# Kernel tuning notes

Hardware: AMD Instinct MI355X
Metric: run time of the kernel (lower is better)

## Reference

```python
import jax, jax.numpy as jnp
import numpy as np
import math

CODE_DIMS = [32, 32]
NUM_CODEBOOK = 16
FEAT_DIM = 1024
EPS = 1e-12


def rms_norm(x, eps=EPS):
    var = jnp.mean(x * x, axis=-1, keepdims=True) + eps
    return x * jax.lax.rsqrt(var)


def outer_product(y, code_dims):
    # y: [..., h, sum(code_dims)] -> [..., h, prod(code_dims)]
    splits = list(np.cumsum(code_dims)[:-1])
    mats = jnp.split(y, splits, axis=-1)
    out = mats[0]
    for m in mats[1:]:
        out = out[..., :, None] * m[..., None, :]
        out = out.reshape(*out.shape[:-2], -1)
    return out


def setup_inputs() -> dict:
    key = jax.random.key(0)
    kx, kw = jax.random.split(key)
    x = jax.random.normal(kx, (4, 2048, FEAT_DIM), dtype=jnp.float32)
    std = math.sqrt(2.0 / (FEAT_DIM + sum(CODE_DIMS)))
    weight = jax.random.normal(kw, (NUM_CODEBOOK, FEAT_DIM, sum(CODE_DIMS)), dtype=jnp.float32) * std
    return {"x": x, "weight": weight}


def reference(x, weight):
    h = weight.shape[0]
    # batched per-codebook linear: [..., d] x [h, d, o] -> [..., h, o]
    y = jnp.einsum('...i,hio->...ho', x, weight)
    # chunked outer product per codebook -> [..., h, prod(code_dims)]
    op = outer_product(y, CODE_DIMS)
    out = jnp.mean(op, axis=-2) * math.sqrt(h)
    return rms_norm(out)
```

## Files before the change

### kernel.cpp

```cpp
#include <hip/hip_runtime.h>
#include <hip/hip_bf16.h>

#define KDIM  1024
#define NOUT  1024
#define NTOK  8192
#define NCB   16
#define BM    256
#define BN    128
#define BK    64
#define BUFSZ 49152
#define NBUF  3

typedef __attribute__((ext_vector_type(8))) short short8;
typedef __attribute__((ext_vector_type(4))) float f32x4;

__device__ static inline unsigned short f2bf(float f) {
    unsigned int u = __float_as_uint(f);
    return (unsigned short)((u + 0x7FFFu + ((u >> 16) & 1u)) >> 16);
}

__device__ static inline float bf2f(unsigned int h) {
    return __uint_as_float(h << 16);
}

__device__ static inline void async_copy16(const void* g, void* l) {
    __builtin_amdgcn_global_load_lds(
        (const __attribute__((address_space(1))) void*)g,
        (__attribute__((address_space(3))) void*)l, 16, 0, 0);
}

__global__ __launch_bounds__(256) void conv_x_kernel(const float* __restrict__ x,
                                                     unsigned short* __restrict__ A) {
    int u = blockIdx.x * 256 + threadIdx.x;
    const float* src = x + (size_t)u * 8;
    float4 v0 = *(const float4*)(src);
    float4 v1 = *(const float4*)(src + 4);
    short8 o;
    o[0] = (short)f2bf(v0.x); o[1] = (short)f2bf(v0.y);
    o[2] = (short)f2bf(v0.z); o[3] = (short)f2bf(v0.w);
    o[4] = (short)f2bf(v1.x); o[5] = (short)f2bf(v1.y);
    o[6] = (short)f2bf(v1.z); o[7] = (short)f2bf(v1.w);
    *(short8*)(A + (size_t)u * 8) = o;
}

__global__ __launch_bounds__(256) void conv_w_kernel(const float* __restrict__ W,
                                                     unsigned short* __restrict__ Bt) {
    int u = blockIdx.x * 256 + threadIdx.x;
    int n  = u & (NOUT - 1);
    int k0 = (u >> 10) << 3;
    int h = n >> 6, o = n & 63;
    const float* src = W + (size_t)h * KDIM * 64 + o;
    short8 v;
#pragma unroll
    for (int j = 0; j < 8; ++j)
        v[j] = (short)f2bf(src[(size_t)(k0 + j) * 64]);
    *(short8*)(Bt + (size_t)n * KDIM + k0) = v;
}

__device__ __forceinline__ void stage_tile(const unsigned short* __restrict__ A,
                                           const unsigned short* __restrict__ Bt,
                                           char* lbase, int tid, int m0, int n0, int kel) {
    unsigned short* Al = (unsigned short*)lbase;
    unsigned short* Bl = (unsigned short*)(lbase + 32768);
#pragma unroll
    for (int i = 0; i < 4; ++i) {
        int s = i * 512 + tid;
        int row = s >> 3;
        int cs = (s & 7) ^ (row & 7);
        async_copy16(A + (size_t)(m0 + row) * KDIM + kel + cs * 8, Al + s * 8);
    }
#pragma unroll
    for (int i = 0; i < 2; ++i) {
        int s = i * 512 + tid;
        int row = s >> 3;
        int cs = (s & 7) ^ (row & 7);
        async_copy16(Bt + (size_t)(n0 + row) * KDIM + kel + cs * 8, Bl + s * 8);
    }
}

template <int VM, bool DO_STAGE>
__device__ __forceinline__ void gemm_step(const unsigned short* __restrict__ A,
                                          const unsigned short* __restrict__ Bt,
                                          char* lds, int tid, int m0, int n0, int kt,
                                          int wm, int wn, int r15, int q,
                                          f32x4 (&acc)[4][4]) {
    if (DO_STAGE)
        stage_tile(A, Bt, lds + ((kt + 2) % NBUF) * BUFSZ, tid, m0, n0, (kt + 2) * BK);
    asm volatile("s_waitcnt vmcnt(%0)" :: "i"(VM) : "memory");
    __builtin_amdgcn_sched_barrier(0);
    __builtin_amdgcn_s_barrier();

    const unsigned short* Al = (const unsigned short*)(lds + (kt % NBUF) * BUFSZ);
    const unsigned short* Bl = (const unsigned short*)(lds + (kt % NBUF) * BUFSZ + 32768);
    short8 af[4][2], bf[4][2];
#pragma unroll
    for (int mf = 0; mf < 4; ++mf)
#pragma unroll
        for (int kk = 0; kk < 2; ++kk) {
            int row = wm * 64 + mf * 16 + r15;
            int c = kk * 4 + q;
            af[mf][kk] = *(const short8*)(Al + row * 64 + ((c ^ (row & 7)) << 3));
        }
#pragma unroll
    for (int nf = 0; nf < 4; ++nf)
#pragma unroll
        for (int kk = 0; kk < 2; ++kk) {
            int row = wn * 64 + nf * 16 + r15;
            int c = kk * 4 + q;
            bf[nf][kk] = *(const short8*)(Bl + row * 64 + ((c ^ (row & 7)) << 3));
        }
    asm volatile("s_waitcnt lgkmcnt(0)" ::: "memory");
    __builtin_amdgcn_sched_barrier(0);
    __builtin_amdgcn_s_barrier();

    __builtin_amdgcn_s_setprio(1);
#pragma unroll
    for (int kk = 0; kk < 2; ++kk)
#pragma unroll
        for (int mf = 0; mf < 4; ++mf)
#pragma unroll
            for (int nf = 0; nf < 4; ++nf)
                acc[mf][nf] = __builtin_amdgcn_mfma_f32_16x16x32_bf16(af[mf][kk], bf[nf][kk], acc[mf][nf], 0, 0, 0);
    __builtin_amdgcn_s_setprio(0);
}

__global__ __launch_bounds__(512, 2) void gemm_kernel(const unsigned short* __restrict__ A,
                                                      const unsigned short* __restrict__ Bt,
                                                      unsigned short* __restrict__ Y) {
    extern __shared__ char lds[];

    const int id  = blockIdx.x;
    const int xcd = id & 7;
    const int j   = id >> 3;
    const int m0  = (xcd * 4 + (j >> 3)) * BM;
    const int n0  = (j & 7) * BN;

    const int tid  = threadIdx.x;
    const int lane = tid & 63;
    const int w    = tid >> 6;
    const int wm   = w >> 1;
    const int wn   = w & 1;
    const int r15  = lane & 15;
    const int q    = lane >> 4;

    f32x4 acc[4][4];
#pragma unroll
    for (int mf = 0; mf < 4; ++mf)
#pragma unroll
        for (int nf = 0; nf < 4; ++nf)
            acc[mf][nf] = (f32x4){0.f, 0.f, 0.f, 0.f};

    stage_tile(A, Bt, lds,         tid, m0, n0, 0);
    stage_tile(A, Bt, lds + BUFSZ, tid, m0, n0, BK);

    for (int kt = 0; kt < 14; ++kt)
        gemm_step<12, true>(A, Bt, lds, tid, m0, n0, kt, wm, wn, r15, q, acc);
    gemm_step<6, false>(A, Bt, lds, tid, m0, n0, 14, wm, wn, r15, q, acc);
    gemm_step<0, false>(A, Bt, lds, tid, m0, n0, 15, wm, wn, r15, q, acc);

#pragma unroll
    for (int mf = 0; mf < 4; ++mf)
#pragma unroll
        for (int nf = 0; nf < 4; ++nf) {
            int col = n0 + wn * 64 + nf * 16 + r15;
#pragma unroll
            for (int r = 0; r < 4; ++r) {
                int row = m0 + wm * 64 + mf * 16 + q * 4 + r;
                Y[(size_t)row * NOUT + col] = f2bf(acc[mf][nf][r]);
            }
        }
}

__global__ __launch_bounds__(256) void epilogue_kernel(const unsigned short* __restrict__ Y,
                                                       float* __restrict__ out) {
    __shared__ float ylds[1024];
    __shared__ float red[4];

    const int t = blockIdx.x;
    const int tid = threadIdx.x;
    const unsigned short* yrow = Y + (size_t)t * NOUT;

    {
        uint2 raw = *(const uint2*)(yrow + tid * 4);
        ylds[tid * 4 + 0] = bf2f(raw.x & 0xffffu);
        ylds[tid * 4 + 1] = bf2f(raw.x >> 16);
        ylds[tid * 4 + 2] = bf2f(raw.y & 0xffffu);
        ylds[tid * 4 + 3] = bf2f(raw.y >> 16);
    }
    __syncthreads();

    const int jj = tid >> 3;
    const int k0 = (tid & 7) * 4;

    float o0 = 0.f, o1 = 0.f, o2 = 0.f, o3 = 0.f;
#pragma unroll
    for (int h = 0; h < NCB; ++h) {
        float a = ylds[h * 64 + jj];
        float4 bb = *(const float4*)&ylds[h * 64 + 32 + k0];
        o0 += a * bb.x; o1 += a * bb.y; o2 += a * bb.z; o3 += a * bb.w;
    }
    o0 *= 0.25f; o1 *= 0.25f; o2 *= 0.25f; o3 *= 0.25f;

    float ss = o0 * o0 + o1 * o1 + o2 * o2 + o3 * o3;
#pragma unroll
    for (int off = 32; off >= 1; off >>= 1)
        ss += __shfl_xor(ss, off, 64);

    const int lane = tid & 63, wv = tid >> 6;
    if (lane == 0) red[wv] = ss;
    __syncthreads();
    float tot = red[0] + red[1] + red[2] + red[3];
    float scale = rsqrtf(tot * (1.0f / 1024.0f) + 1e-12f);

    float4 o;
    o.x = o0 * scale; o.y = o1 * scale; o.z = o2 * scale; o.w = o3 * scale;
    *(float4*)(out + (size_t)t * 1024 + tid * 4) = o;
}

extern "C" void kernel_launch(void* const* d_in, const int* in_sizes, int n_in,
                              void* d_out, int out_size, void* d_ws, size_t ws_size,
                              hipStream_t stream) {
    const float* x   = (const float*)d_in[0];
    const float* wgt = (const float*)d_in[1];
    float* out = (float*)d_out;

    unsigned short* A  = (unsigned short*)d_ws;
    unsigned short* Bt = (unsigned short*)((char*)d_ws + (16u << 20));
    unsigned short* Y  = (unsigned short*)((char*)d_ws + (18u << 20));

    (void)hipFuncSetAttribute((const void*)gemm_kernel,
                              hipFuncAttributeMaxDynamicSharedMemorySize, NBUF * BUFSZ);

    conv_x_kernel<<<NTOK * KDIM / 8 / 256, 256, 0, stream>>>(x, A);
    conv_w_kernel<<<NOUT * KDIM / 8 / 256, 256, 0, stream>>>(wgt, Bt);
    gemm_kernel<<<(NTOK / BM) * (NOUT / BN), 512, NBUF * BUFSZ, stream>>>(A, Bt, Y);
    epilogue_kernel<<<NTOK, 256, 0, stream>>>(Y, out);
}
```

Before: 49.94 us.

## Fuse fp32-to-bf16 conversion of x into GEMM A-tile staging

```diff
diff --git a/kernel.cpp b/kernel.cpp
--- a/kernel.cpp
+++ b/kernel.cpp
@@ -23,24 +23,15 @@
     return __uint_as_float(h << 16);
 }
 
+__device__ static inline unsigned int pk_bf16(float a, float b) {
+    __hip_bfloat162 h = __float22bfloat162_rn(float2{a, b});
+    return *reinterpret_cast<unsigned int*>(&h);
+}
+
 __device__ static inline void async_copy16(const void* g, void* l) {
     __builtin_amdgcn_global_load_lds(
         (const __attribute__((address_space(1))) void*)g,
         (__attribute__((address_space(3))) void*)l, 16, 0, 0);
-}
-
-__global__ __launch_bounds__(256) void conv_x_kernel(const float* __restrict__ x,
-                                                     unsigned short* __restrict__ A) {
-    int u = blockIdx.x * 256 + threadIdx.x;
-    const float* src = x + (size_t)u * 8;
-    float4 v0 = *(const float4*)(src);
-    float4 v1 = *(const float4*)(src + 4);
-    short8 o;
-    o[0] = (short)f2bf(v0.x); o[1] = (short)f2bf(v0.y);
-    o[2] = (short)f2bf(v0.z); o[3] = (short)f2bf(v0.w);
-    o[4] = (short)f2bf(v1.x); o[5] = (short)f2bf(v1.y);
-    o[6] = (short)f2bf(v1.z); o[7] = (short)f2bf(v1.w);
-    *(short8*)(A + (size_t)u * 8) = o;
 }
 
 __global__ __launch_bounds__(256) void conv_w_kernel(const float* __restrict__ W,
@@ -57,18 +48,9 @@
     *(short8*)(Bt + (size_t)n * KDIM + k0) = v;
 }
 
-__device__ __forceinline__ void stage_tile(const unsigned short* __restrict__ A,
-                                           const unsigned short* __restrict__ Bt,
-                                           char* lbase, int tid, int m0, int n0, int kel) {
-    unsigned short* Al = (unsigned short*)lbase;
+__device__ __forceinline__ void stage_b(const unsigned short* __restrict__ Bt,
+                                        char* lbase, int tid, int n0, int kel) {
     unsigned short* Bl = (unsigned short*)(lbase + 32768);
-#pragma unroll
-    for (int i = 0; i < 4; ++i) {
-        int s = i * 512 + tid;
-        int row = s >> 3;
-        int cs = (s & 7) ^ (row & 7);
-        async_copy16(A + (size_t)(m0 + row) * KDIM + kel + cs * 8, Al + s * 8);
-    }
 #pragma unroll
     for (int i = 0; i < 2; ++i) {
         int s = i * 512 + tid;
@@ -78,17 +60,44 @@
     }
 }
 
-template <int VM, bool DO_STAGE>
-__device__ __forceinline__ void gemm_step(const unsigned short* __restrict__ A,
+__device__ __forceinline__ void load_x(const float* __restrict__ x, int tid,
+                                       int m0, int kel, float4 (&rx)[8]) {
+#pragma unroll
+    for (int i = 0; i < 8; ++i) {
+        int idx = i * 512 + tid;
+        int row = idx >> 4, c = idx & 15;
+        rx[i] = *(const float4*)(x + (size_t)(m0 + row) * KDIM + kel + c * 4);
+    }
+}
+
+__device__ __forceinline__ void write_a(char* lbase, int tid, float4 (&rx)[8]) {
+    unsigned short* Al = (unsigned short*)lbase;
+#pragma unroll
+    for (int i = 0; i < 8; ++i) {
+        int idx = i * 512 + tid;
+        int row = idx >> 4, c = idx & 15;
+        uint2 v;
+        v.x = pk_bf16(rx[i].x, rx[i].y);
+        v.y = pk_bf16(rx[i].z, rx[i].w);
+        *(uint2*)(Al + row * 64 + (((c >> 1) ^ (row & 7)) << 3) + ((c & 1) << 2)) = v;
+    }
+}
+
+template <int VM, bool STAGE, bool CONSUME>
+__device__ __forceinline__ void gemm_step(const float* __restrict__ x,
                                           const unsigned short* __restrict__ Bt,
                                           char* lds, int tid, int m0, int n0, int kt,
                                           int wm, int wn, int r15, int q,
+                                          float4 (&rx_fill)[8], float4 (&rx_cons)[8],
                                           f32x4 (&acc)[4][4]) {
-    if (DO_STAGE)
-        stage_tile(A, Bt, lds + ((kt + 2) % NBUF) * BUFSZ, tid, m0, n0, (kt + 2) * BK);
+    if (STAGE) {
+        load_x(x, tid, m0, (kt + 2) * BK, rx_fill);
+        stage_b(Bt, lds + ((kt + 2) % NBUF) * BUFSZ, tid, n0, (kt + 2) * BK);
+    }
     asm volatile("s_waitcnt vmcnt(%0)" :: "i"(VM) : "memory");
     __builtin_amdgcn_sched_barrier(0);
     __builtin_amdgcn_s_barrier();
+    __builtin_amdgcn_sched_barrier(0);
 
     const unsigned short* Al = (const unsigned short*)(lds + (kt % NBUF) * BUFSZ);
     const unsigned short* Bl = (const unsigned short*)(lds + (kt % NBUF) * BUFSZ + 32768);
@@ -109,9 +118,13 @@
             int c = kk * 4 + q;
             bf[nf][kk] = *(const short8*)(Bl + row * 64 + ((c ^ (row & 7)) << 3));
         }
+    if (CONSUME)
+        write_a(lds + ((kt + 1) % NBUF) * BUFSZ, tid, rx_cons);
+
     asm volatile("s_waitcnt lgkmcnt(0)" ::: "memory");
     __builtin_amdgcn_sched_barrier(0);
     __builtin_amdgcn_s_barrier();
+    __builtin_amdgcn_sched_barrier(0);
 
     __builtin_amdgcn_s_setprio(1);
 #pragma unroll
@@ -124,7 +137,7 @@
     __builtin_amdgcn_s_setprio(0);
 }
 
-__global__ __launch_bounds__(512, 2) void gemm_kernel(const unsigned short* __restrict__ A,
+__global__ __launch_bounds__(512, 2) void gemm_kernel(const float* __restrict__ x,
                                                       const unsigned short* __restrict__ Bt,
                                                       unsigned short* __restrict__ Y) {
     extern __shared__ char lds[];
@@ -150,13 +163,26 @@
         for (int nf = 0; nf < 4; ++nf)
             acc[mf][nf] = (f32x4){0.f, 0.f, 0.f, 0.f};
 
-    stage_tile(A, Bt, lds,         tid, m0, n0, 0);
-    stage_tile(A, Bt, lds + BUFSZ, tid, m0, n0, BK);
-
-    for (int kt = 0; kt < 14; ++kt)
-        gemm_step<12, true>(A, Bt, lds, tid, m0, n0, kt, wm, wn, r15, q, acc);
-    gemm_step<6, false>(A, Bt, lds, tid, m0, n0, 14, wm, wn, r15, q, acc);
-    gemm_step<0, false>(A, Bt, lds, tid, m0, n0, 15, wm, wn, r15, q, acc);
+    float4 rxA[8], rxB[8];
+
+    load_x(x, tid, m0, 0, rxA);
+    stage_b(Bt, lds, tid, n0, 0);
+    asm volatile("s_waitcnt vmcnt(2)" ::: "memory");
+    __builtin_amdgcn_sched_barrier(0);
+    write_a(lds, tid, rxA);
+    load_x(x, tid, m0, BK, rxB);
+    stage_b(Bt, lds + BUFSZ, tid, n0, BK);
+    asm volatile("s_waitcnt lgkmcnt(0)" ::: "memory");
+    __builtin_amdgcn_sched_barrier(0);
+    __builtin_amdgcn_s_barrier();
+
+#pragma unroll 1
+    for (int t2 = 0; t2 < 7; ++t2) {
+        gemm_step<12, true, true>(x, Bt, lds, tid, m0, n0, 2 * t2,     wm, wn, r15, q, rxA, rxB, acc);
+        gemm_step<12, true, true>(x, Bt, lds, tid, m0, n0, 2 * t2 + 1, wm, wn, r15, q, rxB, rxA, acc);
+    }
+    gemm_step<2, false, true >(x, Bt, lds, tid, m0, n0, 14, wm, wn, r15, q, rxA, rxB, acc);
+    gemm_step<0, false, false>(x, Bt, lds, tid, m0, n0, 15, wm, wn, r15, q, rxA, rxA, acc);
 
 #pragma unroll
     for (int mf = 0; mf < 4; ++mf)
@@ -224,15 +250,13 @@
     const float* wgt = (const float*)d_in[1];
     float* out = (float*)d_out;
 
-    unsigned short* A  = (unsigned short*)d_ws;
-    unsigned short* Bt = (unsigned short*)((char*)d_ws + (16u << 20));
-    unsigned short* Y  = (unsigned short*)((char*)d_ws + (18u << 20));
+    unsigned short* Bt = (unsigned short*)d_ws;
+    unsigned short* Y  = (unsigned short*)((char*)d_ws + (2u << 20));
 
     (void)hipFuncSetAttribute((const void*)gemm_kernel,
                               hipFuncAttributeMaxDynamicSharedMemorySize, NBUF * BUFSZ);
 
-    conv_x_kernel<<<NTOK * KDIM / 8 / 256, 256, 0, stream>>>(x, A);
     conv_w_kernel<<<NOUT * KDIM / 8 / 256, 256, 0, stream>>>(wgt, Bt);
-    gemm_kernel<<<(NTOK / BM) * (NOUT / BN), 512, NBUF * BUFSZ, stream>>>(A, Bt, Y);
+    gemm_kernel<<<(NTOK / BM) * (NOUT / BN), 512, NBUF * BUFSZ, stream>>>(x, Bt, Y);
     epilogue_kernel<<<NTOK, 256, 0, stream>>>(Y, out);
 }
```

Measured after the change: 55.00 us. 10.1% more time.

## Shrink GEMM tiles to 128x128x32 with 256 threads and fuse conversion kernels

Applied to the files above, without the earlier changes.

```diff
diff --git a/kernel.cpp b/kernel.cpp
--- a/kernel.cpp
+++ b/kernel.cpp
@@ -5,10 +5,10 @@
 #define NOUT  1024
 #define NTOK  8192
 #define NCB   16
-#define BM    256
+#define BM    128
 #define BN    128
-#define BK    64
-#define BUFSZ 49152
+#define BK    32
+#define TILEB 16384
 #define NBUF  3
 
 typedef __attribute__((ext_vector_type(8))) short short8;
@@ -29,102 +29,91 @@
         (__attribute__((address_space(3))) void*)l, 16, 0, 0);
 }
 
-__global__ __launch_bounds__(256) void conv_x_kernel(const float* __restrict__ x,
-                                                     unsigned short* __restrict__ A) {
-    int u = blockIdx.x * 256 + threadIdx.x;
-    const float* src = x + (size_t)u * 8;
-    float4 v0 = *(const float4*)(src);
-    float4 v1 = *(const float4*)(src + 4);
-    short8 o;
-    o[0] = (short)f2bf(v0.x); o[1] = (short)f2bf(v0.y);
-    o[2] = (short)f2bf(v0.z); o[3] = (short)f2bf(v0.w);
-    o[4] = (short)f2bf(v1.x); o[5] = (short)f2bf(v1.y);
-    o[6] = (short)f2bf(v1.z); o[7] = (short)f2bf(v1.w);
-    *(short8*)(A + (size_t)u * 8) = o;
-}
-
-__global__ __launch_bounds__(256) void conv_w_kernel(const float* __restrict__ W,
-                                                     unsigned short* __restrict__ Bt) {
-    int u = blockIdx.x * 256 + threadIdx.x;
-    int n  = u & (NOUT - 1);
-    int k0 = (u >> 10) << 3;
-    int h = n >> 6, o = n & 63;
-    const float* src = W + (size_t)h * KDIM * 64 + o;
-    short8 v;
-#pragma unroll
-    for (int j = 0; j < 8; ++j)
-        v[j] = (short)f2bf(src[(size_t)(k0 + j) * 64]);
-    *(short8*)(Bt + (size_t)n * KDIM + k0) = v;
+__global__ __launch_bounds__(256) void conv_kernel(const float* __restrict__ x,
+                                                   const float* __restrict__ W,
+                                                   unsigned short* __restrict__ A,
+                                                   unsigned short* __restrict__ Bt) {
+    int b = blockIdx.x;
+    if (b < 4096) {
+        int u = b * 256 + threadIdx.x;
+        const float* src = x + (size_t)u * 8;
+        float4 v0 = *(const float4*)(src);
+        float4 v1 = *(const float4*)(src + 4);
+        short8 o;
+        o[0] = (short)f2bf(v0.x); o[1] = (short)f2bf(v0.y);
+        o[2] = (short)f2bf(v0.z); o[3] = (short)f2bf(v0.w);
+        o[4] = (short)f2bf(v1.x); o[5] = (short)f2bf(v1.y);
+        o[6] = (short)f2bf(v1.z); o[7] = (short)f2bf(v1.w);
+        *(short8*)(A + (size_t)u * 8) = o;
+    } else {
+        int u = (b - 4096) * 256 + threadIdx.x;
+        int n  = u & (NOUT - 1);
+        int k0 = (u >> 10) << 3;
+        int h = n >> 6, o = n & 63;
+        const float* src = W + (size_t)h * KDIM * 64 + o;
+        short8 v;
+#pragma unroll
+        for (int j = 0; j < 8; ++j)
+            v[j] = (short)f2bf(src[(size_t)(k0 + j) * 64]);
+        *(short8*)(Bt + (size_t)n * KDIM + k0) = v;
+    }
 }
 
 __device__ __forceinline__ void stage_tile(const unsigned short* __restrict__ A,
                                            const unsigned short* __restrict__ Bt,
                                            char* lbase, int tid, int m0, int n0, int kel) {
     unsigned short* Al = (unsigned short*)lbase;
-    unsigned short* Bl = (unsigned short*)(lbase + 32768);
-#pragma unroll
-    for (int i = 0; i < 4; ++i) {
-        int s = i * 512 + tid;
-        int row = s >> 3;
-        int cs = (s & 7) ^ (row & 7);
-        async_copy16(A + (size_t)(m0 + row) * KDIM + kel + cs * 8, Al + s * 8);
-    }
+    unsigned short* Bl = (unsigned short*)(lbase + 8192);
 #pragma unroll
     for (int i = 0; i < 2; ++i) {
-        int s = i * 512 + tid;
-        int row = s >> 3;
-        int cs = (s & 7) ^ (row & 7);
-        async_copy16(Bt + (size_t)(n0 + row) * KDIM + kel + cs * 8, Bl + s * 8);
-    }
-}
-
-template <int VM, bool DO_STAGE>
+        int s = i * 256 + tid;
+        int row = s >> 2, c = s & 3;
+        async_copy16(A + (size_t)(m0 + row) * KDIM + kel + c * 8, Al + s * 8);
+    }
+#pragma unroll
+    for (int i = 0; i < 2; ++i) {
+        int s = i * 256 + tid;
+        int row = s >> 2, c = s & 3;
+        async_copy16(Bt + (size_t)(n0 + row) * KDIM + kel + c * 8, Bl + s * 8);
+    }
+}
+
+template <int VM, bool STAGE>
 __device__ __forceinline__ void gemm_step(const unsigned short* __restrict__ A,
                                           const unsigned short* __restrict__ Bt,
                                           char* lds, int tid, int m0, int n0, int kt,
-                                          int wm, int wn, int r15, int q,
+                                          int wr, int wc, int r15, int kq,
                                           f32x4 (&acc)[4][4]) {
-    if (DO_STAGE)
-        stage_tile(A, Bt, lds + ((kt + 2) % NBUF) * BUFSZ, tid, m0, n0, (kt + 2) * BK);
+    if (STAGE)
+        stage_tile(A, Bt, lds + ((kt + 2) % NBUF) * TILEB, tid, m0, n0, (kt + 2) * BK);
     asm volatile("s_waitcnt vmcnt(%0)" :: "i"(VM) : "memory");
     __builtin_amdgcn_sched_barrier(0);
     __builtin_amdgcn_s_barrier();
 
-    const unsigned short* Al = (const unsigned short*)(lds + (kt % NBUF) * BUFSZ);
-    const unsigned short* Bl = (const unsigned short*)(lds + (kt % NBUF) * BUFSZ + 32768);
-    short8 af[4][2], bf[4][2];
-#pragma unroll
-    for (int mf = 0; mf < 4; ++mf)
-#pragma unroll
-        for (int kk = 0; kk < 2; ++kk) {
-            int row = wm * 64 + mf * 16 + r15;
-            int c = kk * 4 + q;
-            af[mf][kk] = *(const short8*)(Al + row * 64 + ((c ^ (row & 7)) << 3));
-        }
+    const unsigned short* Al = (const unsigned short*)(lds + (kt % NBUF) * TILEB);
+    const unsigned short* Bl = Al + 4096;
+    short8 af[4], bf[4];
+#pragma unroll
+    for (int mf = 0; mf < 4; ++mf)
+        af[mf] = *(const short8*)(Al + (wr + mf * 16 + r15) * 32 + kq);
 #pragma unroll
     for (int nf = 0; nf < 4; ++nf)
-#pragma unroll
-        for (int kk = 0; kk < 2; ++kk) {
-            int row = wn * 64 + nf * 16 + r15;
-            int c = kk * 4 + q;
-            bf[nf][kk] = *(const short8*)(Bl + row * 64 + ((c ^ (row & 7)) << 3));
-        }
+        bf[nf] = *(const short8*)(Bl + (wc + nf * 16 + r15) * 32 + kq);
+
     asm volatile("s_waitcnt lgkmcnt(0)" ::: "memory");
     __builtin_amdgcn_sched_barrier(0);
     __builtin_amdgcn_s_barrier();
 
     __builtin_amdgcn_s_setprio(1);
 #pragma unroll
-    for (int kk = 0; kk < 2; ++kk)
-#pragma unroll
-        for (int mf = 0; mf < 4; ++mf)
-#pragma unroll
-            for (int nf = 0; nf < 4; ++nf)
-                acc[mf][nf] = __builtin_amdgcn_mfma_f32_16x16x32_bf16(af[mf][kk], bf[nf][kk], acc[mf][nf], 0, 0, 0);
+    for (int mf = 0; mf < 4; ++mf)
+#pragma unroll
+        for (int nf = 0; nf < 4; ++nf)
+            acc[mf][nf] = __builtin_amdgcn_mfma_f32_16x16x32_bf16(af[mf], bf[nf], acc[mf][nf], 0, 0, 0);
     __builtin_amdgcn_s_setprio(0);
 }
 
-__global__ __launch_bounds__(512, 2) void gemm_kernel(const unsigned short* __restrict__ A,
+__global__ __launch_bounds__(256, 3) void gemm_kernel(const unsigned short* __restrict__ A,
                                                       const unsigned short* __restrict__ Bt,
                                                       unsigned short* __restrict__ Y) {
     extern __shared__ char lds[];
@@ -132,16 +121,17 @@
     const int id  = blockIdx.x;
     const int xcd = id & 7;
     const int j   = id >> 3;
-    const int m0  = (xcd * 4 + (j >> 3)) * BM;
+    const int m0  = (xcd * 8 + (j >> 3)) * BM;
     const int n0  = (j & 7) * BN;
 
     const int tid  = threadIdx.x;
     const int lane = tid & 63;
     const int w    = tid >> 6;
-    const int wm   = w >> 1;
-    const int wn   = w & 1;
+    const int wr   = (w >> 1) * 64;
+    const int wc   = (w & 1) * 64;
     const int r15  = lane & 15;
     const int q    = lane >> 4;
+    const int kq   = q * 8;
 
     f32x4 acc[4][4];
 #pragma unroll
@@ -151,21 +141,22 @@
             acc[mf][nf] = (f32x4){0.f, 0.f, 0.f, 0.f};
 
     stage_tile(A, Bt, lds,         tid, m0, n0, 0);
-    stage_tile(A, Bt, lds + BUFSZ, tid, m0, n0, BK);
-
-    for (int kt = 0; kt < 14; ++kt)
-        gemm_step<12, true>(A, Bt, lds, tid, m0, n0, kt, wm, wn, r15, q, acc);
-    gemm_step<6, false>(A, Bt, lds, tid, m0, n0, 14, wm, wn, r15, q, acc);
-    gemm_step<0, false>(A, Bt, lds, tid, m0, n0, 15, wm, wn, r15, q, acc);
+    stage_tile(A, Bt, lds + TILEB, tid, m0, n0, BK);
+
+#pragma unroll 2
+    for (int kt = 0; kt < 30; ++kt)
+        gemm_step<8, true>(A, Bt, lds, tid, m0, n0, kt, wr, wc, r15, kq, acc);
+    gemm_step<4, false>(A, Bt, lds, tid, m0, n0, 30, wr, wc, r15, kq, acc);
+    gemm_step<0, false>(A, Bt, lds, tid, m0, n0, 31, wr, wc, r15, kq, acc);
 
 #pragma unroll
     for (int mf = 0; mf < 4; ++mf)
 #pragma unroll
         for (int nf = 0; nf < 4; ++nf) {
-            int col = n0 + wn * 64 + nf * 16 + r15;
+            int col = n0 + wc + nf * 16 + r15;
 #pragma unroll
             for (int r = 0; r < 4; ++r) {
-                int row = m0 + wm * 64 + mf * 16 + q * 4 + r;
+                int row = m0 + wr + mf * 16 + q * 4 + r;
                 Y[(size_t)row * NOUT + col] = f2bf(acc[mf][nf][r]);
             }
         }
@@ -229,10 +220,9 @@
     unsigned short* Y  = (unsigned short*)((char*)d_ws + (18u << 20));
 
     (void)hipFuncSetAttribute((const void*)gemm_kernel,
-                              hipFuncAttributeMaxDynamicSharedMemorySize, NBUF * BUFSZ);
-
-    conv_x_kernel<<<NTOK * KDIM / 8 / 256, 256, 0, stream>>>(x, A);
-    conv_w_kernel<<<NOUT * KDIM / 8 / 256, 256, 0, stream>>>(wgt, Bt);
-    gemm_kernel<<<(NTOK / BM) * (NOUT / BN), 512, NBUF * BUFSZ, stream>>>(A, Bt, Y);
+                              hipFuncAttributeMaxDynamicSharedMemorySize, NBUF * TILEB);
+
+    conv_kernel<<<4096 + 512, 256, 0, stream>>>(x, wgt, A, Bt);
+    gemm_kernel<<<(NTOK / BM) * (NOUT / BN), 256, NBUF * TILEB, stream>>>(A, Bt, Y);
     epilogue_kernel<<<NTOK, 256, 0, stream>>>(Y, out);
 }
```

Result: no change. 50.00 us (+0.1%).

## Split GEMM k-step into two half-K phases and merge conversion kernels

Applied to the files above, without the earlier changes.

```diff
diff --git a/kernel.cpp b/kernel.cpp
--- a/kernel.cpp
+++ b/kernel.cpp
@@ -8,7 +8,7 @@
 #define BM    256
 #define BN    128
 #define BK    64
-#define BUFSZ 49152
+#define TILEB 49152
 #define NBUF  3
 
 typedef __attribute__((ext_vector_type(8))) short short8;
@@ -29,99 +29,160 @@
         (__attribute__((address_space(3))) void*)l, 16, 0, 0);
 }
 
-__global__ __launch_bounds__(256) void conv_x_kernel(const float* __restrict__ x,
-                                                     unsigned short* __restrict__ A) {
-    int u = blockIdx.x * 256 + threadIdx.x;
-    const float* src = x + (size_t)u * 8;
-    float4 v0 = *(const float4*)(src);
-    float4 v1 = *(const float4*)(src + 4);
-    short8 o;
-    o[0] = (short)f2bf(v0.x); o[1] = (short)f2bf(v0.y);
-    o[2] = (short)f2bf(v0.z); o[3] = (short)f2bf(v0.w);
-    o[4] = (short)f2bf(v1.x); o[5] = (short)f2bf(v1.y);
-    o[6] = (short)f2bf(v1.z); o[7] = (short)f2bf(v1.w);
-    *(short8*)(A + (size_t)u * 8) = o;
-}
-
-__global__ __launch_bounds__(256) void conv_w_kernel(const float* __restrict__ W,
-                                                     unsigned short* __restrict__ Bt) {
-    int u = blockIdx.x * 256 + threadIdx.x;
-    int n  = u & (NOUT - 1);
-    int k0 = (u >> 10) << 3;
-    int h = n >> 6, o = n & 63;
-    const float* src = W + (size_t)h * KDIM * 64 + o;
-    short8 v;
-#pragma unroll
-    for (int j = 0; j < 8; ++j)
-        v[j] = (short)f2bf(src[(size_t)(k0 + j) * 64]);
-    *(short8*)(Bt + (size_t)n * KDIM + k0) = v;
-}
-
-__device__ __forceinline__ void stage_tile(const unsigned short* __restrict__ A,
+__global__ __launch_bounds__(256) void conv_kernel(const float* __restrict__ x,
+                                                   const float* __restrict__ W,
+                                                   unsigned short* __restrict__ A,
+                                                   unsigned short* __restrict__ Bt) {
+    int b = blockIdx.x;
+    if (b < 4096) {
+        int u = b * 256 + threadIdx.x;
+        const float* src = x + (size_t)u * 8;
+        float4 v0 = *(const float4*)(src);
+        float4 v1 = *(const float4*)(src + 4);
+        short8 o;
+        o[0] = (short)f2bf(v0.x); o[1] = (short)f2bf(v0.y);
+        o[2] = (short)f2bf(v0.z); o[3] = (short)f2bf(v0.w);
+        o[4] = (short)f2bf(v1.x); o[5] = (short)f2bf(v1.y);
+        o[6] = (short)f2bf(v1.z); o[7] = (short)f2bf(v1.w);
+        *(short8*)(A + (size_t)u * 8) = o;
+    } else {
+        int u = (b - 4096) * 256 + threadIdx.x;
+        int n  = u & (NOUT - 1);
+        int k0 = (u >> 10) << 3;
+        int h = n >> 6, o = n & 63;
+        const float* src = W + (size_t)h * KDIM * 64 + o;
+        short8 v;
+#pragma unroll
+        for (int j = 0; j < 8; ++j)
+            v[j] = (short)f2bf(src[(size_t)(k0 + j) * 64]);
+        *(short8*)(Bt + (size_t)n * KDIM + k0) = v;
+    }
+}
+
+
+template <int VM, bool STAGE>
+__device__ __forceinline__ void phase0(const unsigned short* __restrict__ A,
+                                       const unsigned short* __restrict__ Bt,
+                                       char* lds, int tid, int m0, int n0, int kt,
+                                       int wm, int wn, int r15, int q,
+                                       f32x4 (&acc)[4][4]) {
+    asm volatile("s_waitcnt vmcnt(%0)" :: "i"(VM) : "memory");
+    __builtin_amdgcn_sched_barrier(0);
+    __builtin_amdgcn_s_barrier();
+    __builtin_amdgcn_sched_barrier(0);
+    if (STAGE) {
+        char* lb = lds + ((kt + 2) % NBUF) * TILEB;
+        unsigned short* Als = (unsigned short*)lb;
+        unsigned short* Bls = (unsigned short*)(lb + 32768);
+        const int kel = (kt + 2) * BK;
+#pragma unroll
+        for (int i = 0; i < 2; ++i) {
+            int s = i * 512 + tid;
+            int row = s >> 3;
+            int cs = (s & 7) ^ (row & 7);
+            async_copy16(A + (size_t)(m0 + row) * KDIM + kel + cs * 8, Als + s * 8);
+        }
+        {
+            int s = tid;
+            int row = s >> 3;
+            int cs = (s & 7) ^ (row & 7);
+            async_copy16(Bt + (size_t)(n0 + row) * KDIM + kel + cs * 8, Bls + s * 8);
+        }
+    }
+    const unsigned short* Al = (const unsigned short*)(lds + (kt % NBUF) * TILEB);
+    const unsigned short* Bl = Al + 16384;
+    short8 af[4], bf[4];
+#pragma unroll
+    for (int mf = 0; mf < 4; ++mf) {
+        int row = wm * 64 + mf * 16 + r15;
+        af[mf] = *(const short8*)(Al + row * 64 + ((q ^ (row & 7)) << 3));
+    }
+#pragma unroll
+    for (int nf = 0; nf < 4; ++nf) {
+        int row = wn * 64 + nf * 16 + r15;
+        bf[nf] = *(const short8*)(Bl + row * 64 + ((q ^ (row & 7)) << 3));
+    }
+    asm volatile("s_waitcnt lgkmcnt(0)" ::: "memory");
+    __builtin_amdgcn_sched_barrier(0);
+    __builtin_amdgcn_s_setprio(1);
+#pragma unroll
+    for (int mf = 0; mf < 4; ++mf)
+#pragma unroll
+        for (int nf = 0; nf < 4; ++nf)
+            acc[mf][nf] = __builtin_amdgcn_mfma_f32_16x16x32_bf16(af[mf], bf[nf], acc[mf][nf], 0, 0, 0);
+    __builtin_amdgcn_s_setprio(0);
+}
+
+template <bool STAGE>
+__device__ __forceinline__ void phase1(const unsigned short* __restrict__ A,
+                                       const unsigned short* __restrict__ Bt,
+                                       char* lds, int tid, int m0, int n0, int kt,
+                                       int wm, int wn, int r15, int q,
+                                       f32x4 (&acc)[4][4]) {
+    __builtin_amdgcn_s_barrier();
+    __builtin_amdgcn_sched_barrier(0);
+    if (STAGE) {
+        char* lb = lds + ((kt + 2) % NBUF) * TILEB;
+        unsigned short* Als = (unsigned short*)lb;
+        unsigned short* Bls = (unsigned short*)(lb + 32768);
+        const int kel = (kt + 2) * BK;
+#pragma unroll
+        for (int i = 2; i < 4; ++i) {
+            int s = i * 512 + tid;
+            int row = s >> 3;
+            int cs = (s & 7) ^ (row & 7);
+            async_copy16(A + (size_t)(m0 + row) * KDIM + kel + cs * 8, Als + s * 8);
+        }
+        {
+            int s = 512 + tid;
+            int row = s >> 3;
+            int cs = (s & 7) ^ (row & 7);
+            async_copy16(Bt + (size_t)(n0 + row) * KDIM + kel + cs * 8, Bls + s * 8);
+        }
+    }
+    const unsigned short* Al = (const unsigned short*)(lds + (kt % NBUF) * TILEB);
+    const unsigned short* Bl = Al + 16384;
+    short8 af[4], bf[4];
+#pragma unroll
+    for (int mf = 0; mf < 4; ++mf) {
+        int row = wm * 64 + mf * 16 + r15;
+        af[mf] = *(const short8*)(Al + row * 64 + (((4 + q) ^ (row & 7)) << 3));
+    }
+#pragma unroll
+    for (int nf = 0; nf < 4; ++nf) {
+        int row = wn * 64 + nf * 16 + r15;
+        bf[nf] = *(const short8*)(Bl + row * 64 + (((4 + q) ^ (row & 7)) << 3));
+    }
+    asm volatile("s_waitcnt lgkmcnt(0)" ::: "memory");
+    __builtin_amdgcn_sched_barrier(0);
+    __builtin_amdgcn_s_setprio(1);
+#pragma unroll
+    for (int mf = 0; mf < 4; ++mf)
+#pragma unroll
+        for (int nf = 0; nf < 4; ++nf)
+            acc[mf][nf] = __builtin_amdgcn_mfma_f32_16x16x32_bf16(af[mf], bf[nf], acc[mf][nf], 0, 0, 0);
+    __builtin_amdgcn_s_setprio(0);
+}
+
+__device__ __forceinline__ void stage_full(const unsigned short* __restrict__ A,
                                            const unsigned short* __restrict__ Bt,
                                            char* lbase, int tid, int m0, int n0, int kel) {
-    unsigned short* Al = (unsigned short*)lbase;
-    unsigned short* Bl = (unsigned short*)(lbase + 32768);
+    unsigned short* Als = (unsigned short*)lbase;
+    unsigned short* Bls = (unsigned short*)(lbase + 32768);
 #pragma unroll
     for (int i = 0; i < 4; ++i) {
         int s = i * 512 + tid;
         int row = s >> 3;
         int cs = (s & 7) ^ (row & 7);
-        async_copy16(A + (size_t)(m0 + row) * KDIM + kel + cs * 8, Al + s * 8);
+        async_copy16(A + (size_t)(m0 + row) * KDIM + kel + cs * 8, Als + s * 8);
     }
 #pragma unroll
     for (int i = 0; i < 2; ++i) {
         int s = i * 512 + tid;
         int row = s >> 3;
         int cs = (s & 7) ^ (row & 7);
-        async_copy16(Bt + (size_t)(n0 + row) * KDIM + kel + cs * 8, Bl + s * 8);
-    }
-}
-
-template <int VM, bool DO_STAGE>
-__device__ __forceinline__ void gemm_step(const unsigned short* __restrict__ A,
-                                          const unsigned short* __restrict__ Bt,
-                                          char* lds, int tid, int m0, int n0, int kt,
-                                          int wm, int wn, int r15, int q,
-                                          f32x4 (&acc)[4][4]) {
-    if (DO_STAGE)
-        stage_tile(A, Bt, lds + ((kt + 2) % NBUF) * BUFSZ, tid, m0, n0, (kt + 2) * BK);
-    asm volatile("s_waitcnt vmcnt(%0)" :: "i"(VM) : "memory");
-    __builtin_amdgcn_sched_barrier(0);
-    __builtin_amdgcn_s_barrier();
-
-    const unsigned short* Al = (const unsigned short*)(lds + (kt % NBUF) * BUFSZ);
-    const unsigned short* Bl = (const unsigned short*)(lds + (kt % NBUF) * BUFSZ + 32768);
-    short8 af[4][2], bf[4][2];
-#pragma unroll
-    for (int mf = 0; mf < 4; ++mf)
-#pragma unroll
-        for (int kk = 0; kk < 2; ++kk) {
-            int row = wm * 64 + mf * 16 + r15;
-            int c = kk * 4 + q;
-            af[mf][kk] = *(const short8*)(Al + row * 64 + ((c ^ (row & 7)) << 3));
-        }
-#pragma unroll
-    for (int nf = 0; nf < 4; ++nf)
-#pragma unroll
-        for (int kk = 0; kk < 2; ++kk) {
-            int row = wn * 64 + nf * 16 + r15;
-            int c = kk * 4 + q;
-            bf[nf][kk] = *(const short8*)(Bl + row * 64 + ((c ^ (row & 7)) << 3));
-        }
-    asm volatile("s_waitcnt lgkmcnt(0)" ::: "memory");
-    __builtin_amdgcn_sched_barrier(0);
-    __builtin_amdgcn_s_barrier();
-
-    __builtin_amdgcn_s_setprio(1);
-#pragma unroll
-    for (int kk = 0; kk < 2; ++kk)
-#pragma unroll
-        for (int mf = 0; mf < 4; ++mf)
-#pragma unroll
-            for (int nf = 0; nf < 4; ++nf)
-                acc[mf][nf] = __builtin_amdgcn_mfma_f32_16x16x32_bf16(af[mf][kk], bf[nf][kk], acc[mf][nf], 0, 0, 0);
-    __builtin_amdgcn_s_setprio(0);
+        async_copy16(Bt + (size_t)(n0 + row) * KDIM + kel + cs * 8, Bls + s * 8);
+    }
 }
 
 __global__ __launch_bounds__(512, 2) void gemm_kernel(const unsigned short* __restrict__ A,
@@ -150,13 +211,18 @@
         for (int nf = 0; nf < 4; ++nf)
             acc[mf][nf] = (f32x4){0.f, 0.f, 0.f, 0.f};
 
-    stage_tile(A, Bt, lds,         tid, m0, n0, 0);
-    stage_tile(A, Bt, lds + BUFSZ, tid, m0, n0, BK);
-
-    for (int kt = 0; kt < 14; ++kt)
-        gemm_step<12, true>(A, Bt, lds, tid, m0, n0, kt, wm, wn, r15, q, acc);
-    gemm_step<6, false>(A, Bt, lds, tid, m0, n0, 14, wm, wn, r15, q, acc);
-    gemm_step<0, false>(A, Bt, lds, tid, m0, n0, 15, wm, wn, r15, q, acc);
+    stage_full(A, Bt, lds,         tid, m0, n0, 0);
+    stage_full(A, Bt, lds + TILEB, tid, m0, n0, BK);
+
+#pragma unroll 1
+    for (int kt = 0; kt < 14; ++kt) {
+        phase0<6, true>(A, Bt, lds, tid, m0, n0, kt, wm, wn, r15, q, acc);
+        phase1<true>   (A, Bt, lds, tid, m0, n0, kt, wm, wn, r15, q, acc);
+    }
+    phase0<6, false>(A, Bt, lds, tid, m0, n0, 14, wm, wn, r15, q, acc);
+    phase1<false>   (A, Bt, lds, tid, m0, n0, 14, wm, wn, r15, q, acc);
+    phase0<0, false>(A, Bt, lds, tid, m0, n0, 15, wm, wn, r15, q, acc);
+    phase1<false>   (A, Bt, lds, tid, m0, n0, 15, wm, wn, r15, q, acc);
 
 #pragma unroll
     for (int mf = 0; mf < 4; ++mf)
@@ -229,10 +295,9 @@
     unsigned short* Y  = (unsigned short*)((char*)d_ws + (18u << 20));
 
     (void)hipFuncSetAttribute((const void*)gemm_kernel,
-                              hipFuncAttributeMaxDynamicSharedMemorySize, NBUF * BUFSZ);
-
-    conv_x_kernel<<<NTOK * KDIM / 8 / 256, 256, 0, stream>>>(x, A);
-    conv_w_kernel<<<NOUT * KDIM / 8 / 256, 256, 0, stream>>>(wgt, Bt);
-    gemm_kernel<<<(NTOK / BM) * (NOUT / BN), 512, NBUF * BUFSZ, stream>>>(A, Bt, Y);
+                              hipFuncAttributeMaxDynamicSharedMemorySize, NBUF * TILEB);
+
+    conv_kernel<<<4096 + 512, 256, 0, stream>>>(x, wgt, A, Bt);
+    gemm_kernel<<<(NTOK / BM) * (NOUT / BN), 512, NBUF * TILEB, stream>>>(A, Bt, Y);
     epilogue_kernel<<<NTOK, 256, 0, stream>>>(Y, out);
 }
```

After: 48.40 us. -3.1%, faster.
